# Kernel tuning notes

Hardware: AMD Instinct MI355X
Metric: run time of the kernel (lower is better)

Reference implementation:

```python
import jax, jax.numpy as jnp
import numpy as np

C = 256

def _conv1x1(x, w, b):
    # x: [B,C,H,W], w: [O,I], b: [O]  (1x1 conv == pointwise GEMM over channels)
    return jnp.einsum('oi,bihw->bohw', w, x) + b[None, :, None, None]

def setup_inputs() -> dict:
    key = jax.random.key(0)
    ks = jax.random.split(key, 9)
    s = 1.0 / np.sqrt(C)
    x = jax.random.normal(ks[0], (16, C, 64, 64), dtype=jnp.float32)
    wf = jax.random.uniform(ks[1], (C, C), jnp.float32, -s, s)
    bf = jax.random.uniform(ks[2], (C,), jnp.float32, -s, s)
    wg = jax.random.uniform(ks[3], (C, C), jnp.float32, -s, s)
    bg = jax.random.uniform(ks[4], (C,), jnp.float32, -s, s)
    wh = jax.random.uniform(ks[5], (C, C), jnp.float32, -s, s)
    bh = jax.random.uniform(ks[6], (C,), jnp.float32, -s, s)
    wv = jax.random.uniform(ks[7], (C, C), jnp.float32, -s, s)
    bv = jax.random.uniform(ks[8], (C,), jnp.float32, -s, s)
    return {"x": x, "wf": wf, "bf": bf, "wg": wg, "bg": bg,
            "wh": wh, "bh": bh, "wv": wv, "bv": bv}

def reference(x, wf, bf, wg, bg, wh, bh, wv, bv):
    fx = _conv1x1(x, wf, bf)              # [B,C,H,W]
    gx = _conv1x1(x, wg, bg)              # [B,C,H,W]
    # scores: fx^T @ gx over spatial H -> [B,C,W,W]
    scores = jnp.einsum('bchw,bchv->bcwv', fx, gx)
    attn = jax.nn.softmax(scores, axis=-1)  # softmax over last W dim
    hx = _conv1x1(x, wh, bh)              # [B,C,H,W]
    out = jnp.einsum('bchw,bcwv->bchv', hx, attn)  # hx @ attn -> [B,C,H,W]
    return _conv1x1(out, wv, bv)
```

## Files before the change

kernel.cpp:

```cpp
#include <hip/hip_runtime.h>
#include <math.h>

#define CH  256
#define SPA 4096
#define BB  16
#define PLANE 16777216

typedef _Float16 f16x8 __attribute__((ext_vector_type(8)));
typedef _Float16 f16x4 __attribute__((ext_vector_type(4)));
typedef float    f32x4 __attribute__((ext_vector_type(4)));

__device__ __forceinline__ void gload16(const void* g, void* l) {
    __builtin_amdgcn_global_load_lds(
        (const __attribute__((address_space(1))) unsigned int*)g,
        (__attribute__((address_space(3))) unsigned int*)l, 16, 0, 0);
}

__global__ __launch_bounds__(256) void xpose_kernel(
    const float* __restrict__ src, _Float16* __restrict__ dst)
{
    __shared__ float T[64][65];
    const int t  = threadIdx.x;
    const int b  = blockIdx.x >> 8;
    const int st = (blockIdx.x >> 2) & 63;
    const int rt = blockIdx.x & 3;
    const int s0 = st << 6, r0 = rt << 6;

    #pragma unroll
    for (int p = 0; p < 4; ++p) {
        int k = (t >> 4) + (p << 4);
        float4 v = *(const float4*)(src + (((size_t)((b << 8) + r0 + k)) << 12)
                                        + s0 + ((t & 15) << 2));
        T[k][((t & 15) << 2) + 0] = v.x;
        T[k][((t & 15) << 2) + 1] = v.y;
        T[k][((t & 15) << 2) + 2] = v.z;
        T[k][((t & 15) << 2) + 3] = v.w;
    }
    __syncthreads();

    const int s  = t >> 2;
    const int kg = (t & 3) << 4;
    const size_t obase = (((size_t)((b << 12) + s0 + s)) << 8) + r0 + kg;

    f16x8 h0, h1;
    #pragma unroll
    for (int i = 0; i < 16; ++i) {
        _Float16 hv = (_Float16)T[kg + i][s];
        if (i < 8) h0[i] = hv; else h1[i - 8] = hv;
    }
    *(f16x8*)(dst + obase)     = h0;
    *(f16x8*)(dst + obase + 8) = h1;
}

__global__ __launch_bounds__(256) void cpose_kernel(
    const _Float16* __restrict__ src, _Float16* __restrict__ dst)
{
    __shared__ _Float16 T[64][68];
    const int t  = threadIdx.x;
    const int b  = blockIdx.x >> 8;
    const int st = (blockIdx.x >> 2) & 63;
    const int ct = blockIdx.x & 3;
    const int s0 = st << 6, c0 = ct << 6;

    #pragma unroll
    for (int p = 0; p < 4; ++p) {
        int fi = (p << 8) + t;
        int r = fi >> 4, s4 = (fi & 15) << 2;
        f16x4 v = *(const f16x4*)(src + (((size_t)((b << 8) + c0 + r)) << 12) + s0 + s4);
        *(f16x4*)&T[r][s4] = v;
    }
    __syncthreads();

    const int s  = t >> 2;
    const int cg = (t & 3) << 4;
    f16x8 h0, h1;
    #pragma unroll
    for (int i = 0; i < 16; ++i) {
        _Float16 hv = T[cg + i][s];
        if (i < 8) h0[i] = hv; else h1[i - 8] = hv;
    }
    const size_t obase = (((size_t)((b << 12) + s0 + s)) << 8) + c0 + cg;
    *(f16x8*)(dst + obase)     = h0;
    *(f16x8*)(dst + obase + 8) = h1;
}

__global__ __launch_bounds__(256) void wcvt_kernel(
    const float* __restrict__ w0, const float* __restrict__ w1,
    const float* __restrict__ w2, const float* __restrict__ w3,
    _Float16* __restrict__ dst)
{
    const int idx = blockIdx.x * 256 + threadIdx.x;
    dst[idx]             = (_Float16)w0[idx];
    dst[65536 + idx]     = (_Float16)w1[idx];
    dst[131072 + idx]    = (_Float16)w2[idx];
    dst[196608 + idx]    = (_Float16)w3[idx];
}

__global__ __launch_bounds__(256, 4) void gemm_fgh_kernel(
    const _Float16* __restrict__ xT, const _Float16* __restrict__ wc,
    const float* __restrict__ bias0, const float* __restrict__ bias1,
    const float* __restrict__ bias2, _Float16* __restrict__ outp)
{
    __shared__ _Float16 S[2][8192];

    const int tid = threadIdx.x;
    const int w = tid >> 6, lane = tid & 63, q = lane >> 4, li = lane & 15;
    const int wx = w & 1, wy = w >> 1;

    const int r_ = ((blockIdx.x & 7) << 9) + (blockIdx.x >> 3);
    const int ot    = r_ & 3;
    const int stile = (r_ >> 2) & 63;
    const int b     = r_ >> 8;
    const int s0 = stile << 6, o0 = ot << 6;

    const float* biases[3] = {bias0, bias1, bias2};

    f32x4 acc[3][2][2];
    #pragma unroll
    for (int m = 0; m < 3; ++m)
        #pragma unroll
        for (int t2 = 0; t2 < 2; ++t2)
            #pragma unroll
            for (int u = 0; u < 2; ++u) acc[m][t2][u] = (f32x4){0.f, 0.f, 0.f, 0.f};

    const int rr = tid >> 2;
    const int cs = (((tid & 3) ^ ((rr >> 1) & 3)) << 3);
    const int sw = (li >> 1) & 3;

    auto STAGE = [&](_Float16* sA, int kb) {
        const size_t ga = (((size_t)((b << 12) + s0 + rr)) << 8) + kb + cs;
        gload16(xT + ga, sA + tid * 8);
        #pragma unroll
        for (int m = 0; m < 3; ++m) {
            const size_t gb = (((size_t)(o0 + rr)) << 8) + m * 65536 + kb + cs;
            gload16(wc + gb, sA + 2048 + m * 2048 + tid * 8);
        }
    };

    auto COMPUTE = [&](const _Float16* sA) {
        f16x8 a[2];
        #pragma unroll
        for (int t2 = 0; t2 < 2; ++t2)
            a[t2] = *(const f16x8*)(sA + (((wy << 5) + (t2 << 4) + li) * 32) + ((q ^ sw) << 3));
        #pragma unroll
        for (int m = 0; m < 3; ++m) {
            const _Float16* sB = sA + 2048 + m * 2048;
            f16x8 b0 = *(const f16x8*)(sB + (((wx << 5) + li) * 32) + ((q ^ sw) << 3));
            f16x8 b1 = *(const f16x8*)(sB + (((wx << 5) + 16 + li) * 32) + ((q ^ sw) << 3));
            #pragma unroll
            for (int t2 = 0; t2 < 2; ++t2) {
                acc[m][t2][0] = __builtin_amdgcn_mfma_f32_16x16x32_f16(a[t2], b0, acc[m][t2][0], 0, 0, 0);
                acc[m][t2][1] = __builtin_amdgcn_mfma_f32_16x16x32_f16(a[t2], b1, acc[m][t2][1], 0, 0, 0);
            }
        }
    };

    STAGE(S[0], 0);

    #pragma unroll 1
    for (int ks = 0; ks < 7; ++ks) {
        STAGE(S[(ks + 1) & 1], (ks + 1) << 5);
        asm volatile("s_waitcnt vmcnt(4)" ::: "memory");
        __builtin_amdgcn_s_barrier();
        COMPUTE(S[ks & 1]);
        asm volatile("s_waitcnt lgkmcnt(0)" ::: "memory");
        __builtin_amdgcn_s_barrier();
    }
    asm volatile("s_waitcnt vmcnt(0)" ::: "memory");
    __builtin_amdgcn_s_barrier();
    COMPUTE(S[1]);

    _Float16* Lr = &S[0][0];
    #pragma unroll
    for (int m = 0; m < 3; ++m) {
        __syncthreads();
        #pragma unroll
        for (int u = 0; u < 2; ++u) {
            const int o = (wx << 5) + (u << 4) + li;
            const float bz = biases[m][o0 + o];
            #pragma unroll
            for (int t2 = 0; t2 < 2; ++t2) {
                const int s = (wy << 5) + (t2 << 4) + (q << 2);
                f32x4 v = acc[m][t2][u];
                f16x4 pv;
                pv[0] = (_Float16)(v[0] + bz); pv[1] = (_Float16)(v[1] + bz);
                pv[2] = (_Float16)(v[2] + bz); pv[3] = (_Float16)(v[3] + bz);
                *(f16x4*)&Lr[o * 72 + s] = pv;
            }
        }
        __syncthreads();
        _Float16* ob = outp + (size_t)m * PLANE;
        #pragma unroll
        for (int it = 0; it < 2; ++it) {
            const int idx = (it << 8) + tid;
            const int row = idx >> 3, c8 = (idx & 7) << 3;
            f16x8 hv = *(const f16x8*)&Lr[row * 72 + c8];
            *(f16x8*)(ob + (((size_t)((b << 8) + o0 + row)) << 12) + s0 + c8) = hv;
        }
    }
}

__global__ __launch_bounds__(256) void gemm16_kernel(
    const _Float16* __restrict__ xT, const _Float16* __restrict__ wp,
    const float* __restrict__ bias, float* __restrict__ outp)
{
    __shared__ _Float16 S[2][8192];

    const int tid = threadIdx.x;
    const int w = tid >> 6, lane = tid & 63, quad = lane >> 4, li = lane & 15;
    const int wx = w & 1, wy = w >> 1;

    const int r_ = ((blockIdx.x & 7) << 7) + (blockIdx.x >> 3);
    const int ot    = r_ & 1;
    const int stile = (r_ >> 1) & 31;
    const int b     = r_ >> 6;
    const int s0 = stile << 7, o0 = ot << 7;

    f32x4 acc[4][4];
    #pragma unroll
    for (int t2 = 0; t2 < 4; ++t2)
        #pragma unroll
        for (int u = 0; u < 4; ++u) acc[t2][u] = (f32x4){0.f, 0.f, 0.f, 0.f};

    const int rr = lane >> 2;
    const int cs = (((lane & 3) ^ ((rr >> 1) & 3)) << 3);
    const int sw = (li >> 1) & 3;

    auto STAGE = [&](_Float16* sAB, int kb) {
        #pragma unroll
        for (int j = 0; j < 32; j += 16) {
            const int r = (w << 5) + j + rr;
            const size_t ga = (((size_t)((b << 12) + s0 + r)) << 8) + kb + cs;
            const size_t gb = ((size_t)(o0 + r) << 8) + kb + cs;
            const int lo_ = ((w << 5) + j) * 32 + lane * 8;
            gload16(xT + ga, sAB + lo_);
            gload16(wp + gb, sAB + 4096 + lo_);
        }
    };

    auto COMPUTE = [&](const _Float16* sAB) {
        f16x8 a[4], bfr[4];
        #pragma unroll
        for (int t2 = 0; t2 < 4; ++t2) {
            a[t2]   = *(const f16x8*)(sAB + ((wy << 6) + (t2 << 4) + li) * 32 + ((quad ^ sw) << 3));
            bfr[t2] = *(const f16x8*)(sAB + 4096 + ((wx << 6) + (t2 << 4) + li) * 32 + ((quad ^ sw) << 3));
        }
        #pragma unroll
        for (int t2 = 0; t2 < 4; ++t2)
            #pragma unroll
            for (int u = 0; u < 4; ++u)
                acc[t2][u] = __builtin_amdgcn_mfma_f32_16x16x32_f16(a[t2], bfr[u], acc[t2][u], 0, 0, 0);
    };

    STAGE(S[0], 0);

    #pragma unroll 1
    for (int ks = 0; ks < 7; ++ks) {
        STAGE(S[(ks + 1) & 1], (ks + 1) << 5);
        asm volatile("s_waitcnt vmcnt(4)" ::: "memory");
        __builtin_amdgcn_s_barrier();
        COMPUTE(S[ks & 1]);
        asm volatile("s_waitcnt lgkmcnt(0)" ::: "memory");
        __builtin_amdgcn_s_barrier();
    }
    asm volatile("s_waitcnt vmcnt(0)" ::: "memory");
    __builtin_amdgcn_s_barrier();
    COMPUTE(S[1]);

    float* Lf = (float*)&S[0][0];
    #pragma unroll
    for (int h = 0; h < 2; ++h) {
        __syncthreads();
        if (wx == h) {
            #pragma unroll
            for (int u = 0; u < 4; ++u) {
                const int r = (u << 4) + li;
                const float bz = bias[o0 + (h << 6) + r];
                #pragma unroll
                for (int t2 = 0; t2 < 4; ++t2) {
                    const int s = (wy << 6) + (t2 << 4) + (quad << 2);
                    f32x4 v = acc[t2][u];
                    f32x4 pv = {v[0] + bz, v[1] + bz, v[2] + bz, v[3] + bz};
                    *(f32x4*)&Lf[r * 128 + (s ^ ((r & 7) << 2))] = pv;
                }
            }
        }
        __syncthreads();
        #pragma unroll
        for (int it = 0; it < 8; ++it) {
            const int idx = (it << 8) + tid;
            const int row = idx >> 5, c4 = (idx & 31) << 2;
            f32x4 v = *(const f32x4*)&Lf[row * 128 + (c4 ^ ((row & 7) << 2))];
            float4 pv = {v[0], v[1], v[2], v[3]};
            *(float4*)(outp + (((size_t)((b << 8) + o0 + (h << 6) + row)) << 12) + s0 + c4) = pv;
        }
    }
}

__global__ __launch_bounds__(256) void attn_mfma_kernel(
    const _Float16* __restrict__ fx, const _Float16* __restrict__ gx,
    const _Float16* __restrict__ hx, _Float16* __restrict__ ob)
{
    __shared__ _Float16 L[23040];
    const int FT = 0, GT = 4608, HM = 9216;
    const int FR = 13824, GR = 18432;
    const int PT = 13824;

    const int t = threadIdx.x;
    const int wave = t >> 6, lane = t & 63, q = lane >> 4, li = lane & 15;
    const int bc = blockIdx.x;
    const _Float16* Fp = fx + (size_t)bc * SPA;
    const _Float16* Gp = gx + (size_t)bc * SPA;
    const _Float16* Hp = hx + (size_t)bc * SPA;
    _Float16* Op = ob + (size_t)bc * SPA;

    #pragma unroll
    for (int p = 0; p < 2; ++p) {
        int ci = t + (p << 8);
        int h = ci >> 3, w8 = (ci & 7) << 3;
        *(f16x8*)&L[FR + h * 72 + w8] = *(const f16x8*)(Fp + h * 64 + w8);
        *(f16x8*)&L[GR + h * 72 + w8] = *(const f16x8*)(Gp + h * 64 + w8);
        *(f16x8*)&L[HM + h * 72 + w8] = *(const f16x8*)(Hp + h * 64 + w8);
    }
    __syncthreads();

    {
        const int src = (wave < 2) ? FR : GR;
        const int dst = (wave < 2) ? FT : GT;
        const int mtb = (wave & 1) << 1;
        f16x8 id0, id1;
        #pragma unroll
        for (int j = 0; j < 8; ++j) {
            id0[j] = (_Float16)(((q << 3) + j == li)      ? 1.0f : 0.0f);
            id1[j] = (_Float16)(((q << 3) + j == li + 16) ? 1.0f : 0.0f);
        }
        #pragma unroll
        for (int mi = 0; mi < 2; ++mi) {
            const int mt = mtb + mi;
            f16x8 a0 = *(const f16x8*)&L[src + (mt * 16 + li) * 72 + (q << 3)];
            f16x8 a1 = *(const f16x8*)&L[src + (mt * 16 + li) * 72 + 32 + (q << 3)];
            #pragma unroll
            for (int nt = 0; nt < 4; ++nt) {
                f32x4 d = {0.f, 0.f, 0.f, 0.f};
                d = __builtin_amdgcn_mfma_f32_16x16x32_f16(
                        (nt < 2) ? a0 : a1, (nt & 1) ? id1 : id0, d, 0, 0, 0);
                f16x4 e;
                e[0] = (_Float16)d[0]; e[1] = (_Float16)d[1];
                e[2] = (_Float16)d[2]; e[3] = (_Float16)d[3];
                *(f16x4*)&L[dst + (nt * 16 + li) * 72 + mt * 16 + (q << 2)] = e;
            }
        }
    }
    __syncthreads();

    {
        f16x8 a0 = *(const f16x8*)&L[FT + (wave * 16 + li) * 72 + (q << 3)];
        f16x8 a1 = *(const f16x8*)&L[FT + (wave * 16 + li) * 72 + 32 + (q << 3)];
        f32x4 s_[4];
        #pragma unroll
        for (int nt = 0; nt < 4; ++nt) {
            f16x8 b0 = *(const f16x8*)&L[GT + (nt * 16 + li) * 72 + (q << 3)];
            f16x8 b1 = *(const f16x8*)&L[GT + (nt * 16 + li) * 72 + 32 + (q << 3)];
            f32x4 acc = {0.f, 0.f, 0.f, 0.f};
            acc = __builtin_amdgcn_mfma_f32_16x16x32_f16(a0, b0, acc, 0, 0, 0);
            acc = __builtin_amdgcn_mfma_f32_16x16x32_f16(a1, b1, acc, 0, 0, 0);
            s_[nt] = acc;
        }
        float mx[4], sm[4];
        #pragma unroll
        for (int r = 0; r < 4; ++r) {
            float m0 = fmaxf(fmaxf(s_[0][r], s_[1][r]), fmaxf(s_[2][r], s_[3][r]));
            m0 = fmaxf(m0, __shfl_xor(m0, 1));
            m0 = fmaxf(m0, __shfl_xor(m0, 2));
            m0 = fmaxf(m0, __shfl_xor(m0, 4));
            m0 = fmaxf(m0, __shfl_xor(m0, 8));
            mx[r] = m0;
        }
        #pragma unroll
        for (int nt = 0; nt < 4; ++nt)
            #pragma unroll
            for (int r = 0; r < 4; ++r)
                s_[nt][r] = __expf(s_[nt][r] - mx[r]);
        #pragma unroll
        for (int r = 0; r < 4; ++r) {
            float s0 = (s_[0][r] + s_[1][r]) + (s_[2][r] + s_[3][r]);
            s0 += __shfl_xor(s0, 1);
            s0 += __shfl_xor(s0, 2);
            s0 += __shfl_xor(s0, 4);
            s0 += __shfl_xor(s0, 8);
            sm[r] = 1.f / s0;
        }
        #pragma unroll
        for (int nt = 0; nt < 4; ++nt) {
            const int v  = nt * 16 + li;
            const int sw = ((v >> 3) & 7) << 3;
            #pragma unroll
            for (int r = 0; r < 4; ++r) {
                const int w = wave * 16 + (q << 2) + r;
                L[PT + v * 72 + (w ^ sw)] = (_Float16)(s_[nt][r] * sm[r]);
            }
        }
    }
    __syncthreads();

    {
        f16x8 a0 = *(const f16x8*)&L[HM + (wave * 16 + li) * 72 + (q << 3)];
        f16x8 a1 = *(const f16x8*)&L[HM + (wave * 16 + li) * 72 + 32 + (q << 3)];
        #pragma unroll
        for (int nt = 0; nt < 4; ++nt) {
            const int v  = nt * 16 + li;
            const int sw = ((v >> 3) & 7) << 3;
            f16x8 b0 = *(const f16x8*)&L[PT + v * 72 + ((q << 3) ^ sw)];
            f16x8 b1 = *(const f16x8*)&L[PT + v * 72 + ((32 + (q << 3)) ^ sw)];
            f32x4 acc = {0.f, 0.f, 0.f, 0.f};
            acc = __builtin_amdgcn_mfma_f32_16x16x32_f16(a0, b0, acc, 0, 0, 0);
            acc = __builtin_amdgcn_mfma_f32_16x16x32_f16(a1, b1, acc, 0, 0, 0);
            #pragma unroll
            for (int r = 0; r < 4; ++r)
                Op[(wave * 16 + (q << 2) + r) * 64 + v] = (_Float16)acc[r];
        }
    }
}

extern "C" void kernel_launch(void* const* d_in, const int* in_sizes, int n_in,
                              void* d_out, int out_size, void* d_ws, size_t ws_size,
                              hipStream_t stream)
{
    const float* x  = (const float*)d_in[0];
    const float* wf = (const float*)d_in[1];
    const float* bf = (const float*)d_in[2];
    const float* wg = (const float*)d_in[3];
    const float* bg = (const float*)d_in[4];
    const float* wh = (const float*)d_in[5];
    const float* bh = (const float*)d_in[6];
    const float* wv = (const float*)d_in[7];
    const float* bv = (const float*)d_in[8];

    char* base = (char*)d_ws;
    const size_t MB = 1ull << 20;
    _Float16* xT  = (_Float16*)base;
    _Float16* fxb = (_Float16*)(base + 32 * MB);
    _Float16* ob  = (_Float16*)(base + 128 * MB);
    _Float16* obT = (_Float16*)base;
    _Float16* wc  = (_Float16*)(base + 160 * MB);

    _Float16* gxb = fxb + PLANE;
    _Float16* hxb = gxb + PLANE;

    dim3 blk(256);
    xpose_kernel<<<4096, blk, 0, stream>>>(x, xT);
    wcvt_kernel<<<256, blk, 0, stream>>>(wf, wg, wh, wv, wc);

    gemm_fgh_kernel<<<4096, blk, 0, stream>>>(xT, wc, bf, bg, bh, fxb);

    attn_mfma_kernel<<<4096, blk, 0, stream>>>(fxb, gxb, hxb, ob);

    cpose_kernel<<<4096, blk, 0, stream>>>(ob, obT);

    gemm16_kernel<<<1024, blk, 0, stream>>>(obT, wc + 196608, bv, (float*)d_out);
}
```

Before: 247.5 us.

## Fuse input transpose and fp16 conversion into the f/g/h projection GEMM

Removes the separate transpose kernel that turned fp32 x into an fp16 spatial-major copy. The fused f/g/h GEMM now stages raw fp32 x tiles in channel-major order straight into LDS through async global-to-LDS loads. It then builds the fp16 A fragments with strided scalar LDS reads and in-register conversion. This drops one full read-write pass over the input. The cost is more global bytes per GEMM tile, a larger LDS footprint per block, and scalar, possibly bank-conflicting LDS reads in the inner loop.

```diff
diff --git a/kernel.cpp b/kernel.cpp
--- a/kernel.cpp
+++ b/kernel.cpp
@@ -14,42 +14,6 @@
     __builtin_amdgcn_global_load_lds(
         (const __attribute__((address_space(1))) unsigned int*)g,
         (__attribute__((address_space(3))) unsigned int*)l, 16, 0, 0);
-}
-
-__global__ __launch_bounds__(256) void xpose_kernel(
-    const float* __restrict__ src, _Float16* __restrict__ dst)
-{
-    __shared__ float T[64][65];
-    const int t  = threadIdx.x;
-    const int b  = blockIdx.x >> 8;
-    const int st = (blockIdx.x >> 2) & 63;
-    const int rt = blockIdx.x & 3;
-    const int s0 = st << 6, r0 = rt << 6;
-
-    #pragma unroll
-    for (int p = 0; p < 4; ++p) {
-        int k = (t >> 4) + (p << 4);
-        float4 v = *(const float4*)(src + (((size_t)((b << 8) + r0 + k)) << 12)
-                                        + s0 + ((t & 15) << 2));
-        T[k][((t & 15) << 2) + 0] = v.x;
-        T[k][((t & 15) << 2) + 1] = v.y;
-        T[k][((t & 15) << 2) + 2] = v.z;
-        T[k][((t & 15) << 2) + 3] = v.w;
-    }
-    __syncthreads();
-
-    const int s  = t >> 2;
-    const int kg = (t & 3) << 4;
-    const size_t obase = (((size_t)((b << 12) + s0 + s)) << 8) + r0 + kg;
-
-    f16x8 h0, h1;
-    #pragma unroll
-    for (int i = 0; i < 16; ++i) {
-        _Float16 hv = (_Float16)T[kg + i][s];
-        if (i < 8) h0[i] = hv; else h1[i - 8] = hv;
-    }
-    *(f16x8*)(dst + obase)     = h0;
-    *(f16x8*)(dst + obase + 8) = h1;
 }
 
 __global__ __launch_bounds__(256) void cpose_kernel(
@@ -97,11 +61,11 @@
 }
 
 __global__ __launch_bounds__(256, 4) void gemm_fgh_kernel(
-    const _Float16* __restrict__ xT, const _Float16* __restrict__ wc,
+    const float* __restrict__ x, const _Float16* __restrict__ wc,
     const float* __restrict__ bias0, const float* __restrict__ bias1,
     const float* __restrict__ bias2, _Float16* __restrict__ outp)
 {
-    __shared__ _Float16 S[2][8192];
+    __shared__ char SS[2][20480];
 
     const int tid = threadIdx.x;
     const int w = tid >> 6, lane = tid & 63, q = lane >> 4, li = lane & 15;
@@ -127,24 +91,34 @@
     const int cs = (((tid & 3) ^ ((rr >> 1) & 3)) << 3);
     const int sw = (li >> 1) & 3;
 
-    auto STAGE = [&](_Float16* sA, int kb) {
-        const size_t ga = (((size_t)((b << 12) + s0 + rr)) << 8) + kb + cs;
-        gload16(xT + ga, sA + tid * 8);
+    auto STAGE = [&](char* buf, int kb) {
+        float* xf = (float*)buf;
+        _Float16* sB = (_Float16*)(buf + 8192);
+        const size_t gx1 = (((size_t)((b << 8) + kb + (tid >> 4))) << 12)
+                           + s0 + ((tid & 15) << 2);
+        gload16(x + gx1, xf + tid * 4);
+        gload16(x + gx1 + (16ull << 12), xf + 1024 + tid * 4);
         #pragma unroll
         for (int m = 0; m < 3; ++m) {
             const size_t gb = (((size_t)(o0 + rr)) << 8) + m * 65536 + kb + cs;
-            gload16(wc + gb, sA + 2048 + m * 2048 + tid * 8);
+            gload16(wc + gb, sB + m * 2048 + tid * 8);
         }
     };
 
-    auto COMPUTE = [&](const _Float16* sA) {
+    auto COMPUTE = [&](const char* buf) {
+        const float* xf = (const float*)buf;
+        const _Float16* sBb = (const _Float16*)(buf + 8192);
         f16x8 a[2];
         #pragma unroll
-        for (int t2 = 0; t2 < 2; ++t2)
-            a[t2] = *(const f16x8*)(sA + (((wy << 5) + (t2 << 4) + li) * 32) + ((q ^ sw) << 3));
+        for (int t2 = 0; t2 < 2; ++t2) {
+            const int r = (wy << 5) + (t2 << 4) + li;
+            #pragma unroll
+            for (int j = 0; j < 8; ++j)
+                a[t2][j] = (_Float16)xf[(((q << 3) + j) << 6) + r];
+        }
         #pragma unroll
         for (int m = 0; m < 3; ++m) {
-            const _Float16* sB = sA + 2048 + m * 2048;
+            const _Float16* sB = sBb + m * 2048;
             f16x8 b0 = *(const f16x8*)(sB + (((wx << 5) + li) * 32) + ((q ^ sw) << 3));
             f16x8 b1 = *(const f16x8*)(sB + (((wx << 5) + 16 + li) * 32) + ((q ^ sw) << 3));
             #pragma unroll
@@ -155,22 +129,22 @@
         }
     };
 
-    STAGE(S[0], 0);
+    STAGE(SS[0], 0);
 
     #pragma unroll 1
     for (int ks = 0; ks < 7; ++ks) {
-        STAGE(S[(ks + 1) & 1], (ks + 1) << 5);
-        asm volatile("s_waitcnt vmcnt(4)" ::: "memory");
+        STAGE(SS[(ks + 1) & 1], (ks + 1) << 5);
+        asm volatile("s_waitcnt vmcnt(5)" ::: "memory");
         __builtin_amdgcn_s_barrier();
-        COMPUTE(S[ks & 1]);
+        COMPUTE(SS[ks & 1]);
         asm volatile("s_waitcnt lgkmcnt(0)" ::: "memory");
         __builtin_amdgcn_s_barrier();
     }
     asm volatile("s_waitcnt vmcnt(0)" ::: "memory");
     __builtin_amdgcn_s_barrier();
-    COMPUTE(S[1]);
-
-    _Float16* Lr = &S[0][0];
+    COMPUTE(SS[1]);
+
+    _Float16* Lr = (_Float16*)&SS[0][0];
     #pragma unroll
     for (int m = 0; m < 3; ++m) {
         __syncthreads();
@@ -438,7 +412,6 @@
 
     char* base = (char*)d_ws;
     const size_t MB = 1ull << 20;
-    _Float16* xT  = (_Float16*)base;
     _Float16* fxb = (_Float16*)(base + 32 * MB);
     _Float16* ob  = (_Float16*)(base + 128 * MB);
     _Float16* obT = (_Float16*)base;
@@ -448,10 +421,9 @@
     _Float16* hxb = gxb + PLANE;
 
     dim3 blk(256);
-    xpose_kernel<<<4096, blk, 0, stream>>>(x, xT);
     wcvt_kernel<<<256, blk, 0, stream>>>(wf, wg, wh, wv, wc);
 
-    gemm_fgh_kernel<<<4096, blk, 0, stream>>>(xT, wc, bf, bg, bh, fxb);
+    gemm_fgh_kernel<<<4096, blk, 0, stream>>>(x, wc, bf, bg, bh, fxb);
 
     attn_mfma_kernel<<<4096, blk, 0, stream>>>(fxb, gxb, hxb, ob);
 
```

Result: slower. 254.0 us (+2.6%).
